# Kernel optimization log

Hardware: AMD Instinct MI355X
Metric: run time of the kernel (lower is better)

The kernel has to match this reference:

```python
import jax, jax.numpy as jnp
import numpy as np

N_TOPICS = 1024
TOPIC_DIM = 128
HIDDEN = 512
N_HEADS = 8
HEAD_DIM = HIDDEN // N_HEADS
N_LAYERS = 2
ALPHA = 0.2
TIME_DECAY = 0.1
BATCH = 8


def setup_inputs() -> dict:
    key = jax.random.key(0)
    ks = jax.random.split(key, 16)
    inp = {
        'topic_ids': jax.random.randint(ks[0], (BATCH,), 0, N_TOPICS, dtype=jnp.int32),
        'adj_matrix': jax.random.randint(ks[1], (BATCH, N_TOPICS, N_TOPICS), 0, 2, dtype=jnp.int32),
        'time_matrix': jax.random.uniform(ks[2], (BATCH, N_TOPICS, N_TOPICS), dtype=jnp.float32),
        'attractiveness': jax.random.normal(ks[3], (BATCH,), dtype=jnp.float32),
        # parameters (torch Linear convention: W [out,in], y = x@W.T + b)
        'topic_embedding': jax.random.normal(ks[4], (N_TOPICS, TOPIC_DIM), dtype=jnp.float32) * 0.1,
        'struct_W': jax.random.normal(ks[5], (HIDDEN, TOPIC_DIM), dtype=jnp.float32) * 0.05,
        'struct_b': jnp.zeros((HIDDEN,), dtype=jnp.float32),
        'attract_W': jax.random.normal(ks[6], (HIDDEN, 1), dtype=jnp.float32) * 0.05,
        'attract_b': jnp.zeros((HIDDEN,), dtype=jnp.float32),
        'gat_W': jax.random.normal(ks[7], (N_LAYERS, N_HEADS, HIDDEN, HEAD_DIM), dtype=jnp.float32) * 0.05,
        'gat_a': jax.random.normal(ks[8], (N_LAYERS, N_HEADS, 2 * HEAD_DIM, 1), dtype=jnp.float32) * 0.05,
        'fc1_W': jax.random.normal(ks[9], (HIDDEN, HIDDEN), dtype=jnp.float32) * 0.05,
        'fc1_b': jnp.zeros((HIDDEN,), dtype=jnp.float32),
        'fc2_W': jax.random.normal(ks[10], (1, HIDDEN), dtype=jnp.float32) * 0.05,
        'fc2_b': jnp.zeros((1,), dtype=jnp.float32),
    }
    return inp


def _gat_layer(node, adj, time_w, W, a):
    # node: [B,N,F], adj: [B,N,N] (0/1), time_w: [B,N,N]
    # W: [H,F,hd], a: [H,2*hd,1]
    h = jnp.einsum('bni,hio->bhno', node, W)  # [B,H,N,hd]
    # Additive attention: a = [a_src; a_dst] so e_ij = LeakyReLU(h_i.a_src + h_j.a_dst)
    a_src = a[:, :HEAD_DIM, 0]   # [H,hd]
    a_dst = a[:, HEAD_DIM:, 0]   # [H,hd]
    e_src = jnp.einsum('bhnd,hd->bhn', h, a_src)  # [B,H,N]
    e_dst = jnp.einsum('bhnd,hd->bhn', h, a_dst)  # [B,H,N]
    e = e_src[:, :, :, None] + e_dst[:, :, None, :]  # [B,H,N,N]
    e = jax.nn.leaky_relu(e, negative_slope=ALPHA)
    e = e * time_w[:, None, :, :]
    e = jnp.where(adj[:, None, :, :] == 0, -jnp.inf, e)
    attn = jax.nn.softmax(e, axis=-1)
    out = jnp.einsum('bhij,bhjd->bhid', attn, h)  # [B,H,N,hd]
    out = out.transpose(0, 2, 1, 3).reshape(node.shape[0], node.shape[1], -1)
    return jax.nn.elu(out)


def reference(topic_ids, adj_matrix, time_matrix, attractiveness,
              topic_embedding, struct_W, struct_b, attract_W, attract_b,
              gat_W, gat_a, fc1_W, fc1_b, fc2_W, fc2_b):
    # structural features for all topics -> hidden
    struct = topic_embedding @ struct_W.T + struct_b          # [N,hidden]
    attract = attractiveness[:, None] @ attract_W.T + attract_b  # [B,hidden]
    node = jnp.broadcast_to(struct[None], (BATCH, N_TOPICS, HIDDEN))
    # weighted co-occurrence time (eq.17)
    time_w = jnp.exp(-TIME_DECAY * (time_matrix.max() - time_matrix))  # [B,N,N]
    for l in range(N_LAYERS):
        node = _gat_layer(node, adj_matrix, time_w, gat_W[l], gat_a[l])
    # gather per-sample topic node feature
    topic_feat = jnp.take_along_axis(node, topic_ids[:, None, None].astype(jnp.int32), axis=1)[:, 0]  # [B,hidden]
    combined = topic_feat + attract
    hidden = jax.nn.relu(combined @ fc1_W.T + fc1_b)
    pred = hidden @ fc2_W.T + fc2_b  # [B,1]
    return pred
```

## Files before the change

kernel.cpp:

```cpp
#include <hip/hip_runtime.h>

#define NT 1024
#define TD 128
#define HID 512
#define NH 8
#define HD 64
#define NB 8

typedef unsigned short us;
typedef _Float16 h16;
typedef h16 half8 __attribute__((ext_vector_type(8)));
typedef h16 h16x2 __attribute__((ext_vector_type(2)));
typedef float f32x4 __attribute__((ext_vector_type(4)));

#define LOG2E 1.44269504f

extern "C" __device__ _Float16 __ocml_exp2_f16(_Float16);

__device__ __forceinline__ us f2h(float x) { return __builtin_bit_cast(us, (h16)x); }
__device__ __forceinline__ float h2f(us s) { return (float)__builtin_bit_cast(h16, s); }
__device__ __forceinline__ unsigned int pkh2(float a, float b) {
    auto v = __builtin_amdgcn_cvt_pkrtz(a, b);
    return __builtin_bit_cast(unsigned int, v);
}

__global__ __launch_bounds__(256) void kprep(const float* __restrict__ tm, const int* __restrict__ adj,
                                             float* __restrict__ part, us* __restrict__ TWb,
                                             const float* __restrict__ emb, const float* __restrict__ sW,
                                             const float* __restrict__ sb, us* __restrict__ node0b,
                                             const float* __restrict__ gW, us* __restrict__ Wt,
                                             const float* __restrict__ fc2b, float* __restrict__ out) {
    __shared__ __align__(16) float smf[8768];
    int bx = blockIdx.x, t = threadIdx.x;
    if (bx < 1024) {
        const float4* tm4 = (const float4*)tm;
        const int4* ad4 = (const int4*)adj;
        size_t base = (size_t)bx * 256 + t;
        const float C = 0.1f * LOG2E;
        const float NANF = __uint_as_float(0x7FC00000u);
        float m = -1e30f;
        #pragma unroll
        for (int k = 0; k < 8; k++) {
            size_t fi = base + (size_t)k * 262144;
            float4 v = tm4[fi];
            int4 av = ad4[fi];
            m = fmaxf(m, fmaxf(fmaxf(v.x, v.y), fmaxf(v.z, v.w)));
            float w0 = exp2f(v.x * C) * LOG2E;
            float w1 = exp2f(v.y * C) * LOG2E;
            float w2 = exp2f(v.z * C) * LOG2E;
            float w3 = exp2f(v.w * C) * LOG2E;
            w0 = av.x ? w0 : NANF;
            w1 = av.y ? w1 : NANF;
            w2 = av.z ? w2 : NANF;
            w3 = av.w ? w3 : NANF;
            uint2 pk;
            pk.x = pkh2(w0, w1);
            pk.y = pkh2(w2, w3);
            *(uint2*)&TWb[fi * 4] = pk;
        }
        smf[t] = m; __syncthreads();
        for (int s = 128; s > 0; s >>= 1) { if (t < s) smf[t] = fmaxf(smf[t], smf[t + s]); __syncthreads(); }
        if (t == 0) part[bx] = smf[0];
    } else if (bx < 1152) {
        int g = bx - 1024; int iblk = g & 15, oseg = g >> 4;
        us* As = (us*)smf;
        us* Bs = (us*)smf + 64 * 136;
        const float4* esrc = (const float4*)(emb + (size_t)iblk * 64 * TD);
        const float4* wsrc = (const float4*)(sW + (size_t)oseg * 64 * TD);
        #pragma unroll
        for (int rep = 0; rep < 8; rep++) {
            int f = rep * 256 + t;
            int row = f >> 5, c4 = f & 31;
            float4 av = esrc[f];
            float4 bv = wsrc[f];
            uint2 pa, pb;
            pa.x = pkh2(av.x, av.y); pa.y = pkh2(av.z, av.w);
            pb.x = pkh2(bv.x, bv.y); pb.y = pkh2(bv.z, bv.w);
            *(uint2*)&As[row * 136 + c4 * 4] = pa;
            *(uint2*)&Bs[row * 136 + c4 * 4] = pb;
        }
        __syncthreads();
        int l = t & 63, w = t >> 6, m = l & 15, q = l >> 4;
        f32x4 acc[4];
        #pragma unroll
        for (int ot = 0; ot < 4; ot++) acc[ot] = (f32x4){0.f, 0.f, 0.f, 0.f};
        #pragma unroll
        for (int ks = 0; ks < 4; ks++) {
            half8 a = *(const half8*)&As[(w * 16 + m) * 136 + ks * 32 + q * 8];
            #pragma unroll
            for (int ot = 0; ot < 4; ot++) {
                half8 b = *(const half8*)&Bs[(ot * 16 + m) * 136 + ks * 32 + q * 8];
                acc[ot] = __builtin_amdgcn_mfma_f32_16x16x32_f16(a, b, acc[ot], 0, 0, 0);
            }
        }
        #pragma unroll
        for (int ot = 0; ot < 4; ot++) {
            int col = oseg * 64 + ot * 16 + m;
            float sbv = sb[col];
            #pragma unroll
            for (int rr = 0; rr < 4; rr++) {
                int rowi = iblk * 64 + w * 16 + q * 4 + rr;
                node0b[(size_t)rowi * HID + col] = f2h(acc[ot][rr] + sbv);
            }
        }
    } else {
        int g = bx - 1152; int lh = g >> 3, kt = g & 7;
        if (g == 0 && t < NB) out[t] = fc2b[0];
        float* tile = smf;
        const float4* src = (const float4*)(gW + ((size_t)lh * HID + kt * 64) * HD);
        #pragma unroll
        for (int rep = 0; rep < 4; rep++) {
            int f = rep * 256 + t;
            float4 v = src[f];
            int row = f >> 4, col = (f & 15) * 4;
            float* d = tile + row * 65 + col;
            d[0] = v.x; d[1] = v.y; d[2] = v.z; d[3] = v.w;
        }
        __syncthreads();
        int o = t >> 2, ks = (t & 3) * 16;
        us pk[16];
        #pragma unroll
        for (int j = 0; j < 16; j++) pk[j] = f2h(tile[(ks + j) * 65 + o]);
        us* dst = Wt + (size_t)lh * HD * HID + (size_t)o * HID + kt * 64 + ks;
        *(uint4*)dst = *(uint4*)pk;
        *(uint4*)(dst + 8) = *(uint4*)&pk[8];
    }
}

__device__ __forceinline__ void gemm_body(const us* __restrict__ A, const us* __restrict__ W,
                                          const float* __restrict__ gav,
                                          us* __restrict__ outT, us* __restrict__ outR,
                                          float* __restrict__ esO, float* __restrict__ edO,
                                          int iblk, int b, int h, int t, us* sm) {
    us* As = sm;
    us* Bs = sm + 2 * 4608;
    int row = t >> 2, ks = t & 3;
    int l = t & 63, w = t >> 6, m = l & 15, q = l >> 4;
    size_t arow0 = (size_t)(b * NT + iblk * 64);
    const us* ar = A + (arow0 + row) * HID + ks * 16;
    const us* br = W + ((size_t)(h * HD + row)) * HID + ks * 16;
    f32x4 acc[4];
    #pragma unroll
    for (int ot = 0; ot < 4; ot++) acc[ot] = (f32x4){0.f, 0.f, 0.f, 0.f};
    {
        uint4 x0 = *(const uint4*)ar, x1 = *(const uint4*)(ar + 8);
        uint4 y0 = *(const uint4*)br, y1 = *(const uint4*)(br + 8);
        *(uint4*)&As[row * 72 + ks * 16] = x0; *(uint4*)&As[row * 72 + ks * 16 + 8] = x1;
        *(uint4*)&Bs[row * 72 + ks * 16] = y0; *(uint4*)&Bs[row * 72 + ks * 16 + 8] = y1;
    }
    uint4 a0 = *(const uint4*)(ar + 64), a1 = *(const uint4*)(ar + 72);
    uint4 b0 = *(const uint4*)(br + 64), b1 = *(const uint4*)(br + 72);
    for (int it = 0; it < 8; it++) {
        int cur = it & 1, nxt = cur ^ 1;
        uint4 na0, na1, nb0, nb1;
        if (it < 6) {
            int k0 = (it + 2) * 64;
            na0 = *(const uint4*)(ar + k0); na1 = *(const uint4*)(ar + k0 + 8);
            nb0 = *(const uint4*)(br + k0); nb1 = *(const uint4*)(br + k0 + 8);
        }
        __syncthreads();
        if (it < 7) {
            *(uint4*)&As[nxt * 4608 + row * 72 + ks * 16] = a0;
            *(uint4*)&As[nxt * 4608 + row * 72 + ks * 16 + 8] = a1;
            *(uint4*)&Bs[nxt * 4608 + row * 72 + ks * 16] = b0;
            *(uint4*)&Bs[nxt * 4608 + row * 72 + ks * 16 + 8] = b1;
        }
        const us* Ac = As + cur * 4608; const us* Bc = Bs + cur * 4608;
        #pragma unroll
        for (int kt = 0; kt < 2; kt++) {
            half8 av = *(const half8*)&Ac[(w * 16 + m) * 72 + kt * 32 + q * 8];
            #pragma unroll
            for (int ot = 0; ot < 4; ot++) {
                half8 bv = *(const half8*)&Bc[(ot * 16 + m) * 72 + kt * 32 + q * 8];
                acc[ot] = __builtin_amdgcn_mfma_f32_16x16x32_f16(av, bv, acc[ot], 0, 0, 0);
            }
        }
        if (it < 6) { a0 = na0; a1 = na1; b0 = nb0; b1 = nb1; }
    }
    const float* gas = gav + h * 2 * HD;
    float gs[4], gd[4];
    #pragma unroll
    for (int ot = 0; ot < 4; ot++) { gs[ot] = gas[ot * 16 + m]; gd[ot] = gas[HD + ot * 16 + m]; }
    size_t ebase = ((size_t)b * NH + h) * NT + iblk * 64;
    #pragma unroll
    for (int rr = 0; rr < 4; rr++) {
        float s = 0.f, d = 0.f;
        #pragma unroll
        for (int ot = 0; ot < 4; ot++) { float v = acc[ot][rr]; s = fmaf(v, gs[ot], s); d = fmaf(v, gd[ot], d); }
        #pragma unroll
        for (int mask = 1; mask < 16; mask <<= 1) { s += __shfl_xor(s, mask); d += __shfl_xor(d, mask); }
        if (m == 0) {
            int rowi = w * 16 + q * 4 + rr;
            esO[ebase + rowi] = s;
            edO[ebase + rowi] = d;
        }
    }
    #pragma unroll
    for (int ot = 0; ot < 4; ot++) {
        int col = h * HD + ot * 16 + m;
        #pragma unroll
        for (int rr = 0; rr < 4; rr++) {
            int i_loc = w * 16 + q * 4 + rr;
            float v = acc[ot][rr];
            if (outT) outT[(size_t)col * NT + iblk * 64 + i_loc] = f2h(v);
            if (outR) outR[(arow0 + i_loc) * HID + col] = f2h(v);
        }
    }
}

__global__ __launch_bounds__(256) void kgemm1(const us* __restrict__ node0b, const us* __restrict__ Wt,
                                              const float* __restrict__ ga, us* __restrict__ Ht1,
                                              float* __restrict__ es1, float* __restrict__ ed1) {
    __shared__ __align__(16) us sm[4 * 4608];
    int g = blockIdx.x;
    gemm_body(node0b, Wt, ga, Ht1, nullptr, es1, ed1, g & 15, 0, g >> 4, threadIdx.x, sm);
}

__global__ __launch_bounds__(256) void kgemm2(const us* __restrict__ node1b, const us* __restrict__ Wt2,
                                              const float* __restrict__ ga2, us* __restrict__ H2b,
                                              float* __restrict__ es2, float* __restrict__ ed2) {
    __shared__ __align__(16) us sm[4 * 4608];
    int n = blockIdx.x;
    int b = n & 7, k = n >> 3, iblk = k & 15, h = k >> 4;
    gemm_body(node1b, Wt2, ga2, nullptr, H2b, es2, ed2, iblk, b, h, threadIdx.x, sm);
}

__device__ __forceinline__ unsigned int p_word_fly(unsigned int tw, unsigned int ed, h16x2 es) {
    h16x2 t = __builtin_bit_cast(h16x2, tw);
    h16x2 d = __builtin_bit_cast(h16x2, ed);
    h16x2 e = es + d;
    h16x2 lk = e * (h16)0.2f;
    h16x2 el = __builtin_elementwise_max(e, lk);
    h16x2 mm = t * el;
    h16x2 p;
    p.x = __ocml_exp2_f16(mm.x);
    p.y = __ocml_exp2_f16(mm.y);
    h16x2 z = {(h16)0.0f, (h16)0.0f};
    h16x2 r = __builtin_elementwise_max(p, z);
    return __builtin_bit_cast(unsigned int, r);
}

__device__ __forceinline__ half8 p_frag(uint4 T, uint4 D, h16x2 es) {
    uint4 r;
    r.x = p_word_fly(T.x, D.x, es);
    r.y = p_word_fly(T.y, D.y, es);
    r.z = p_word_fly(T.z, D.z, es);
    r.w = p_word_fly(T.w, D.w, es);
    return __builtin_bit_cast(half8, r);
}

__global__ __launch_bounds__(256) void kattn1(const us* __restrict__ TWb, const us* __restrict__ Ht,
                                              const float* __restrict__ es1, const float* __restrict__ ed1,
                                              const float* __restrict__ part, us* __restrict__ node1b) {
    int n = blockIdx.x;
    int b = n & 7, k = n >> 3;
    int i2 = k & 7, h = k >> 3;
    int t = threadIdx.x;
    __shared__ __align__(16) us Hs[2][64 * 72];
    __shared__ __align__(16) us edl[NT];
    __shared__ float invl_s[128];
    __shared__ float reds[256];
    int l = t & 63, w = t >> 6, m = l & 15, q = l >> 4;
    {
        float pm = fmaxf(fmaxf(part[t * 4], part[t * 4 + 1]), fmaxf(part[t * 4 + 2], part[t * 4 + 3]));
        reds[t] = pm; __syncthreads();
        for (int s = 128; s > 0; s >>= 1) { if (t < s) reds[t] = fmaxf(reds[t], reds[t + s]); __syncthreads(); }
    }
    float sfac = exp2f(-reds[0] * (0.1f * LOG2E));
    {
        float4 ev = *(const float4*)&ed1[h * NT + t * 4];
        uint2 pk; pk.x = pkh2(ev.x * sfac, ev.y * sfac); pk.y = pkh2(ev.z * sfac, ev.w * sfac);
        *(uint2*)&edl[t * 4] = pk;
    }
    int rowA = i2 * 128 + w * 32 + m;
    h16 eA = (h16)(es1[h * NT + rowA] * sfac);
    h16 eB = (h16)(es1[h * NT + rowA + 16] * sfac);
    h16x2 esvA = {eA, eA}, esvB = {eB, eB};
    const us* twA = TWb + ((size_t)(b * NT) + rowA) * NT + q * 8;
    const us* twB = twA + (size_t)16 * NT;
    int hr = t >> 2, js = t & 3;
    const us* htrow = Ht + ((size_t)(h * HD) + hr) * NT + js * 16;
    f32x4 acc[2][4];
    #pragma unroll
    for (int ti = 0; ti < 2; ti++)
        #pragma unroll
        for (int ot = 0; ot < 4; ot++) acc[ti][ot] = (f32x4){0.f, 0.f, 0.f, 0.f};
    f32x4 acc1[2] = {(f32x4){0.f, 0.f, 0.f, 0.f}, (f32x4){0.f, 0.f, 0.f, 0.f}};
    h16 ov = (m == 0) ? (h16)1.0f : (h16)0.0f;
    half8 bones = {ov, ov, ov, ov, ov, ov, ov, ov};
    uint4 H0 = *(const uint4*)htrow, H1 = *(const uint4*)(htrow + 8);
    *(uint4*)&Hs[0][hr * 72 + js * 16] = H0;
    *(uint4*)&Hs[0][hr * 72 + js * 16 + 8] = H1;
    H0 = *(const uint4*)(htrow + 64); H1 = *(const uint4*)(htrow + 72);
    uint4 TA0 = *(const uint4*)twA,        TA1 = *(const uint4*)(twA + 32);
    uint4 TB0 = *(const uint4*)twB,        TB1 = *(const uint4*)(twB + 32);
    __syncthreads();
    for (int it = 0; it < 16; it++) {
        int cur = it & 1, nxt = cur ^ 1;
        int j0 = it * 64;
        uint4 nH0, nH1, nA0, nA1, nB0, nB1;
        if (it < 14) {
            nH0 = *(const uint4*)(htrow + j0 + 128);
            nH1 = *(const uint4*)(htrow + j0 + 136);
        }
        if (it < 15) {
            nA0 = *(const uint4*)(twA + j0 + 64);  nA1 = *(const uint4*)(twA + j0 + 96);
            nB0 = *(const uint4*)(twB + j0 + 64);  nB1 = *(const uint4*)(twB + j0 + 96);
        }
        uint4 D0 = *(const uint4*)&edl[j0 + q * 8];
        uint4 D1 = *(const uint4*)&edl[j0 + 32 + q * 8];
        half8 pA0 = p_frag(TA0, D0, esvA);
        half8 pA1 = p_frag(TA1, D1, esvA);
        half8 pB0 = p_frag(TB0, D0, esvB);
        half8 pB1 = p_frag(TB1, D1, esvB);
        __syncthreads();
        if (it < 15) {
            *(uint4*)&Hs[nxt][hr * 72 + js * 16] = H0;
            *(uint4*)&Hs[nxt][hr * 72 + js * 16 + 8] = H1;
        }
        const us* Hc = Hs[cur];
        #pragma unroll
        for (int ot = 0; ot < 4; ot++) {
            half8 bv0 = *(const half8*)&Hc[(ot * 16 + m) * 72 + q * 8];
            half8 bv1 = *(const half8*)&Hc[(ot * 16 + m) * 72 + 32 + q * 8];
            acc[0][ot] = __builtin_amdgcn_mfma_f32_16x16x32_f16(pA0, bv0, acc[0][ot], 0, 0, 0);
            acc[0][ot] = __builtin_amdgcn_mfma_f32_16x16x32_f16(pA1, bv1, acc[0][ot], 0, 0, 0);
            acc[1][ot] = __builtin_amdgcn_mfma_f32_16x16x32_f16(pB0, bv0, acc[1][ot], 0, 0, 0);
            acc[1][ot] = __builtin_amdgcn_mfma_f32_16x16x32_f16(pB1, bv1, acc[1][ot], 0, 0, 0);
        }
        acc1[0] = __builtin_amdgcn_mfma_f32_16x16x32_f16(pA0, bones, acc1[0], 0, 0, 0);
        acc1[0] = __builtin_amdgcn_mfma_f32_16x16x32_f16(pA1, bones, acc1[0], 0, 0, 0);
        acc1[1] = __builtin_amdgcn_mfma_f32_16x16x32_f16(pB0, bones, acc1[1], 0, 0, 0);
        acc1[1] = __builtin_amdgcn_mfma_f32_16x16x32_f16(pB1, bones, acc1[1], 0, 0, 0);
        if (it < 14) { H0 = nH0; H1 = nH1; }
        if (it < 15) { TA0 = nA0; TA1 = nA1; TB0 = nB0; TB1 = nB1; }
    }
    if (m == 0) {
        #pragma unroll
        for (int rr = 0; rr < 4; rr++) {
            invl_s[w * 32 + q * 4 + rr]      = 1.f / acc1[0][rr];
            invl_s[w * 32 + 16 + q * 4 + rr] = 1.f / acc1[1][rr];
        }
    }
    __syncthreads();
    size_t rbase = (size_t)(b * NT + i2 * 128);
    #pragma unroll
    for (int ti = 0; ti < 2; ti++) {
        #pragma unroll
        for (int ot = 0; ot < 4; ot++) {
            int col = h * HD + ot * 16 + m;
            #pragma unroll
            for (int rr = 0; rr < 4; rr++) {
                int rloc = w * 32 + ti * 16 + q * 4 + rr;
                float v = acc[ti][ot][rr] * invl_s[rloc];
                v = v > 0.f ? v : (__expf(v) - 1.f);
                node1b[(rbase + rloc) * HID + col] = f2h(v);
            }
        }
    }
}

__global__ __launch_bounds__(256) void kattn2a(const us* __restrict__ TWb, const us* __restrict__ H2b,
                                               const float* __restrict__ es2, const float* __restrict__ ed2,
                                               const int* __restrict__ topic_ids, const float* __restrict__ part,
                                               float* __restrict__ ppv, float* __restrict__ pl) {
    int js = blockIdx.x, h = blockIdx.y, b = blockIdx.z;
    int t = threadIdx.x;
    __shared__ float pls[64];
    __shared__ float red[256];
    int qi = topic_ids[b];
    {
        float pm = fmaxf(fmaxf(part[t * 4], part[t * 4 + 1]), fmaxf(part[t * 4 + 2], part[t * 4 + 3]));
        red[t] = pm; __syncthreads();
        for (int s = 128; s > 0; s >>= 1) { if (t < s) red[t] = fmaxf(red[t], red[t + s]); __syncthreads(); }
    }
    float sfac = exp2f(-red[0] * (0.1f * LOG2E));
    __syncthreads();
    if (t < 64) {
        int j = js * 64 + t;
        float esq = es2[((size_t)b * NH + h) * NT + qi];
        float tw = h2f(TWb[((size_t)(b * NT) + qi) * NT + j]);
        float e = esq + ed2[((size_t)b * NH + h) * NT + j];
        e = fmaxf(e, 0.2f * e) * (tw * sfac);
        float p = fmaxf(exp2f(e), 0.f);
        pls[t] = p;
        float lsum = p;
        #pragma unroll
        for (int mask = 1; mask < 64; mask <<= 1) lsum += __shfl_xor(lsum, mask);
        if (t == 0) pl[((size_t)b * NH + h) * 16 + js] = lsum;
    }
    __syncthreads();
    int o = t & 63, jg = t >> 6;
    float acc = 0.f;
    const us* hb = H2b + ((size_t)(b * NT) + js * 64 + jg * 16) * HID + h * HD + o;
    #pragma unroll
    for (int jj = 0; jj < 16; jj++)
        acc = fmaf(pls[jg * 16 + jj], h2f(hb[(size_t)jj * HID]), acc);
    red[t] = acc; __syncthreads();
    if (t < 64) {
        float pv = red[t] + red[t + 64] + red[t + 128] + red[t + 192];
        ppv[(((size_t)b * NH + h) * 16 + js) * HD + t] = pv;
    }
}

__global__ __launch_bounds__(256) void khead2(const float* __restrict__ ppv, const float* __restrict__ pl,
                                              const float* __restrict__ attr,
                                              const float* __restrict__ aW, const float* __restrict__ ab,
                                              const float* __restrict__ fc1W, const float* __restrict__ fc1b,
                                              const float* __restrict__ fc2W, float* __restrict__ out) {
    int kseg = blockIdx.x, b = blockIdx.y;
    int t = threadIdx.x;
    __shared__ float comb[HID];
    __shared__ float linv[NH];
    __shared__ float r2[256];
    if (t < NH) {
        float lsum = 0.f;
        #pragma unroll
        for (int js = 0; js < 16; js++) lsum += pl[((size_t)b * NH + t) * 16 + js];
        linv[t] = 1.f / lsum;
    }
    __syncthreads();
    float av = attr[b];
    for (int k = t; k < HID; k += 256) {
        int h = k >> 6, o = k & 63;
        float pv = 0.f;
        #pragma unroll
        for (int js = 0; js < 16; js++) pv += ppv[(((size_t)b * NH + h) * 16 + js) * HD + o];
        float v = pv * linv[h];
        v = v > 0.f ? v : (__expf(v) - 1.f);
        comb[k] = v + av * aW[k] + ab[k];
    }
    __syncthreads();
    int kk = kseg * 16 + (t >> 4);
    int j = t & 15;
    const float* row = fc1W + (size_t)kk * HID;
    float acc = 0.f;
    #pragma unroll 8
    for (int mi = 0; mi < 32; mi++) {
        int idx = mi * 16 + j;
        acc = fmaf(comb[idx], row[idx], acc);
    }
    #pragma unroll
    for (int mask = 1; mask < 16; mask <<= 1) acc += __shfl_xor(acc, mask);
    float partv = 0.f;
    if (j == 0) {
        float hk = fmaxf(acc + fc1b[kk], 0.f);
        partv = hk * fc2W[kk];
    }
    r2[t] = partv; __syncthreads();
    for (int s = 128; s > 0; s >>= 1) { if (t < s) r2[t] += r2[t + s]; __syncthreads(); }
    if (t == 0) atomicAdd(&out[b], r2[0]);
}

extern "C" void kernel_launch(void* const* d_in, const int* in_sizes, int n_in,
                              void* d_out, int out_size, void* d_ws, size_t ws_size,
                              hipStream_t stream) {
    const int*   topic_ids = (const int*)d_in[0];
    const int*   adj       = (const int*)d_in[1];
    const float* tm        = (const float*)d_in[2];
    const float* attr      = (const float*)d_in[3];
    const float* emb       = (const float*)d_in[4];
    const float* sW        = (const float*)d_in[5];
    const float* sb        = (const float*)d_in[6];
    const float* aW        = (const float*)d_in[7];
    const float* ab        = (const float*)d_in[8];
    const float* gW        = (const float*)d_in[9];
    const float* ga        = (const float*)d_in[10];
    const float* fc1W      = (const float*)d_in[11];
    const float* fc1b      = (const float*)d_in[12];
    const float* fc2W      = (const float*)d_in[13];
    const float* fc2b      = (const float*)d_in[14];
    float* out = (float*)d_out;

    char* p = (char*)d_ws;
    us* TWb    = (us*)p; p += sizeof(us) * (size_t)NB * NT * NT;
    us* node0b = (us*)p; p += sizeof(us) * (size_t)NT * HID;
    us* Wt     = (us*)p; p += sizeof(us) * (size_t)2 * NH * HD * HID;
    us* Ht1    = (us*)p; p += sizeof(us) * (size_t)HID * NT;
    us* node1b = (us*)p; p += sizeof(us) * (size_t)NB * NT * HID;
    us* H2b    = (us*)p; p += sizeof(us) * (size_t)NB * NT * HID;
    float* es1  = (float*)p; p += sizeof(float) * NH * NT;
    float* ed1  = (float*)p; p += sizeof(float) * NH * NT;
    float* es2  = (float*)p; p += sizeof(float) * NB * NH * NT;
    float* ed2  = (float*)p; p += sizeof(float) * NB * NH * NT;
    float* ppv  = (float*)p; p += sizeof(float) * NB * NH * 16 * HD;
    float* pl   = (float*)p; p += sizeof(float) * NB * NH * 16;
    float* part = (float*)p; p += sizeof(float) * 1024;

    kprep<<<1280, 256, 0, stream>>>(tm, adj, part, TWb, emb, sW, sb, node0b, gW, Wt, fc2b, out);
    kgemm1<<<128, 256, 0, stream>>>(node0b, Wt, ga, Ht1, es1, ed1);
    kattn1<<<512, 256, 0, stream>>>(TWb, Ht1, es1, ed1, part, node1b);
    kgemm2<<<1024, 256, 0, stream>>>(node1b, Wt + (size_t)NH * HD * HID,
                                     ga + NH * 2 * HD, H2b, es2, ed2);
    kattn2a<<<dim3(16, NH, NB), 256, 0, stream>>>(TWb, H2b, es2, ed2, topic_ids, part, ppv, pl);
    khead2<<<dim3(32, NB), 256, 0, stream>>>(ppv, pl, attr, aW, ab, fc1W, fc1b, fc2W, out);
}
```

Before: 179.3 us.

## Reassociate layer-2 attention to skip full per-batch GEMM for query row

Layer 2 only feeds one query row per batch, so the full per-batch GEMM H2 = node1 @ W2 is dropped. The attention scores are rebuilt from node1 dotted with the precomputed vectors W2·a_src and W2·a_dst, and the projection is applied after the attention-weighted sum of node1 rows (context then W2). This removes a large GEMM and the H2 write and read, in exchange for new kctx/kcomb/kfc kernels and an extra 64-block section in kprep.

Measured after the change: 175.9 us (median of 2 runs). Within noise of the previous version (-1.9%).

```diff
diff --git a/kernel.cpp b/kernel.cpp
--- a/kernel.cpp
+++ b/kernel.cpp
@@ -29,6 +29,7 @@
                                              const float* __restrict__ emb, const float* __restrict__ sW,
                                              const float* __restrict__ sb, us* __restrict__ node0b,
                                              const float* __restrict__ gW, us* __restrict__ Wt,
+                                             const float* __restrict__ ga, us* __restrict__ VAVS,
                                              const float* __restrict__ fc2b, float* __restrict__ out) {
     __shared__ __align__(16) float smf[8768];
     int bx = blockIdx.x, t = threadIdx.x;
@@ -103,7 +104,7 @@
                 node0b[(size_t)rowi * HID + col] = f2h(acc[ot][rr] + sbv);
             }
         }
-    } else {
+    } else if (bx < 1280) {
         int g = bx - 1152; int lh = g >> 3, kt = g & 7;
         if (g == 0 && t < NB) out[t] = fc2b[0];
         float* tile = smf;
@@ -124,12 +125,25 @@
         us* dst = Wt + (size_t)lh * HD * HID + (size_t)o * HID + kt * 64 + ks;
         *(uint4*)dst = *(uint4*)pk;
         *(uint4*)(dst + 8) = *(uint4*)&pk[8];
+    } else {
+        int g = bx - 1280; int h = g >> 3, iseg = g & 7;
+        if (t < 128) {
+            int sel = t >> 6, il = t & 63;
+            int i = iseg * 64 + il;
+            const float* W2row = gW + (size_t)NH * HID * HD + ((size_t)h * HID + i) * HD;
+            const float* a2 = ga + NH * 2 * HD + h * 2 * HD;
+            const float* av = sel ? a2 : (a2 + HD);
+            float s = 0.f;
+            #pragma unroll 8
+            for (int o = 0; o < HD; o++) s = fmaf(W2row[o], av[o], s);
+            VAVS[(size_t)(sel * 8 + h) * HID + i] = f2h(s);
+        }
     }
 }
 
 __device__ __forceinline__ void gemm_body(const us* __restrict__ A, const us* __restrict__ W,
                                           const float* __restrict__ gav,
-                                          us* __restrict__ outT, us* __restrict__ outR,
+                                          us* __restrict__ outT,
                                           float* __restrict__ esO, float* __restrict__ edO,
                                           int iblk, int b, int h, int t, us* sm) {
     us* As = sm;
@@ -201,9 +215,7 @@
         #pragma unroll
         for (int rr = 0; rr < 4; rr++) {
             int i_loc = w * 16 + q * 4 + rr;
-            float v = acc[ot][rr];
-            if (outT) outT[(size_t)col * NT + iblk * 64 + i_loc] = f2h(v);
-            if (outR) outR[(arow0 + i_loc) * HID + col] = f2h(v);
+            outT[(size_t)col * NT + iblk * 64 + i_loc] = f2h(acc[ot][rr]);
         }
     }
 }
@@ -213,16 +225,7 @@
                                               float* __restrict__ es1, float* __restrict__ ed1) {
     __shared__ __align__(16) us sm[4 * 4608];
     int g = blockIdx.x;
-    gemm_body(node0b, Wt, ga, Ht1, nullptr, es1, ed1, g & 15, 0, g >> 4, threadIdx.x, sm);
-}
-
-__global__ __launch_bounds__(256) void kgemm2(const us* __restrict__ node1b, const us* __restrict__ Wt2,
-                                              const float* __restrict__ ga2, us* __restrict__ H2b,
-                                              float* __restrict__ es2, float* __restrict__ ed2) {
-    __shared__ __align__(16) us sm[4 * 4608];
-    int n = blockIdx.x;
-    int b = n & 7, k = n >> 3, iblk = k & 15, h = k >> 4;
-    gemm_body(node1b, Wt2, ga2, nullptr, H2b, es2, ed2, iblk, b, h, threadIdx.x, sm);
+    gemm_body(node0b, Wt, ga, Ht1, es1, ed1, g & 15, 0, g >> 4, threadIdx.x, sm);
 }
 
 __device__ __forceinline__ unsigned int p_word_fly(unsigned int tw, unsigned int ed, h16x2 es) {
@@ -360,76 +363,156 @@
     }
 }
 
-__global__ __launch_bounds__(256) void kattn2a(const us* __restrict__ TWb, const us* __restrict__ H2b,
-                                               const float* __restrict__ es2, const float* __restrict__ ed2,
-                                               const int* __restrict__ topic_ids, const float* __restrict__ part,
-                                               float* __restrict__ ppv, float* __restrict__ pl) {
-    int js = blockIdx.x, h = blockIdx.y, b = blockIdx.z;
+__global__ __launch_bounds__(256) void kctx(const us* __restrict__ TWb, const us* __restrict__ node1b,
+                                            const us* __restrict__ VAVS, const float* __restrict__ part,
+                                            const int* __restrict__ topic_ids,
+                                            float* __restrict__ ctxp, float* __restrict__ pl) {
+    int n = blockIdx.x;
+    int b = n & 7, jb = n >> 3;
     int t = threadIdx.x;
-    __shared__ float pls[64];
-    __shared__ float red[256];
+    __shared__ __align__(16) us n1s[32 * 520];
+    __shared__ __align__(16) us vvs[16 * 520];
+    __shared__ __align__(16) us qrow[HID];
+    __shared__ float Ps[8][33];
+    __shared__ float es2q[8];
+    __shared__ float reds[256];
     int qi = topic_ids[b];
     {
         float pm = fmaxf(fmaxf(part[t * 4], part[t * 4 + 1]), fmaxf(part[t * 4 + 2], part[t * 4 + 3]));
-        red[t] = pm; __syncthreads();
-        for (int s = 128; s > 0; s >>= 1) { if (t < s) red[t] = fmaxf(red[t], red[t + s]); __syncthreads(); }
-    }
-    float sfac = exp2f(-red[0] * (0.1f * LOG2E));
-    __syncthreads();
-    if (t < 64) {
-        int j = js * 64 + t;
-        float esq = es2[((size_t)b * NH + h) * NT + qi];
-        float tw = h2f(TWb[((size_t)(b * NT) + qi) * NT + j]);
-        float e = esq + ed2[((size_t)b * NH + h) * NT + j];
-        e = fmaxf(e, 0.2f * e) * (tw * sfac);
-        float p = fmaxf(exp2f(e), 0.f);
-        pls[t] = p;
-        float lsum = p;
-        #pragma unroll
-        for (int mask = 1; mask < 64; mask <<= 1) lsum += __shfl_xor(lsum, mask);
-        if (t == 0) pl[((size_t)b * NH + h) * 16 + js] = lsum;
-    }
-    __syncthreads();
-    int o = t & 63, jg = t >> 6;
-    float acc = 0.f;
-    const us* hb = H2b + ((size_t)(b * NT) + js * 64 + jg * 16) * HID + h * HD + o;
-    #pragma unroll
-    for (int jj = 0; jj < 16; jj++)
-        acc = fmaf(pls[jg * 16 + jj], h2f(hb[(size_t)jj * HID]), acc);
-    red[t] = acc; __syncthreads();
-    if (t < 64) {
-        float pv = red[t] + red[t + 64] + red[t + 128] + red[t + 192];
-        ppv[(((size_t)b * NH + h) * 16 + js) * HD + t] = pv;
-    }
-}
-
-__global__ __launch_bounds__(256) void khead2(const float* __restrict__ ppv, const float* __restrict__ pl,
-                                              const float* __restrict__ attr,
-                                              const float* __restrict__ aW, const float* __restrict__ ab,
-                                              const float* __restrict__ fc1W, const float* __restrict__ fc1b,
-                                              const float* __restrict__ fc2W, float* __restrict__ out) {
+        reds[t] = pm; __syncthreads();
+        for (int s = 128; s > 0; s >>= 1) { if (t < s) reds[t] = fmaxf(reds[t], reds[t + s]); __syncthreads(); }
+    }
+    float sfac = exp2f(-reds[0] * (0.1f * LOG2E));
+    {
+        int row = t >> 3, c = (t & 7) * 64;
+        const uint4* src = (const uint4*)(node1b + ((size_t)(b * NT) + jb * 32 + row) * HID + c);
+        uint4* dst = (uint4*)&n1s[row * 520 + c];
+        #pragma unroll
+        for (int k = 0; k < 8; k++) dst[k] = src[k];
+    }
+    {
+        int row = t >> 4, c = (t & 15) * 32;
+        const uint4* src = (const uint4*)(VAVS + (size_t)row * HID + c);
+        uint4* dst = (uint4*)&vvs[row * 520 + c];
+        dst[0] = src[0]; dst[1] = src[1]; dst[2] = src[2]; dst[3] = src[3];
+    }
+    if (t < 32) {
+        const uint4* src = (const uint4*)(node1b + ((size_t)(b * NT) + qi) * HID + t * 16);
+        *(uint4*)&qrow[t * 16] = src[0];
+        *(uint4*)&qrow[t * 16 + 8] = src[1];
+    }
+    __syncthreads();
+    {
+        int h = t >> 5, li = t & 31;
+        float s = 0.f;
+        #pragma unroll 4
+        for (int ii = 0; ii < 16; ii++) {
+            int i = li * 16 + ii;
+            s = fmaf(h2f(qrow[i]), h2f(vvs[(8 + h) * 520 + i]), s);
+        }
+        #pragma unroll
+        for (int mask = 1; mask < 32; mask <<= 1) s += __shfl_xor(s, mask);
+        if (li == 0) es2q[h] = s;
+    }
+    __syncthreads();
+    int l = t & 63, w = t >> 6, m = l & 15, q = l >> 4;
+    if (w < 2) {
+        f32x4 acc = (f32x4){0.f, 0.f, 0.f, 0.f};
+        #pragma unroll
+        for (int kt = 0; kt < 16; kt++) {
+            half8 a = *(const half8*)&n1s[(w * 16 + m) * 520 + kt * 32 + q * 8];
+            half8 bv = *(const half8*)&vvs[m * 520 + kt * 32 + q * 8];
+            acc = __builtin_amdgcn_mfma_f32_16x16x32_f16(a, bv, acc, 0, 0, 0);
+        }
+        if (m < 8) {
+            const us* twq = TWb + ((size_t)(b * NT) + qi) * NT + jb * 32;
+            float esv = es2q[m];
+            #pragma unroll
+            for (int r = 0; r < 4; r++) {
+                int j = w * 16 + q * 4 + r;
+                float e = esv + acc[r];
+                e = fmaxf(e, 0.2f * e);
+                float twu = h2f(twq[j]);
+                float p = fmaxf(exp2f(twu * sfac * e), 0.f);
+                Ps[m][j] = p;
+            }
+        }
+    }
+    __syncthreads();
+    {
+        int h = t >> 5, j = t & 31;
+        float s = Ps[h][j];
+        #pragma unroll
+        for (int mask = 1; mask < 32; mask <<= 1) s += __shfl_xor(s, mask);
+        if (j == 0) pl[((size_t)b * NH + h) * 32 + jb] = s;
+    }
+    float ac[8][2];
+    #pragma unroll
+    for (int h = 0; h < 8; h++) { ac[h][0] = 0.f; ac[h][1] = 0.f; }
+    for (int j = 0; j < 32; j++) {
+        unsigned int uv = *(const unsigned int*)&n1s[j * 520 + t * 2];
+        h16x2 hv = __builtin_bit_cast(h16x2, uv);
+        float f0 = (float)hv.x, f1 = (float)hv.y;
+        #pragma unroll
+        for (int h = 0; h < 8; h++) {
+            float p = Ps[h][j];
+            ac[h][0] = fmaf(p, f0, ac[h][0]);
+            ac[h][1] = fmaf(p, f1, ac[h][1]);
+        }
+    }
+    float* cp = ctxp + (((size_t)b * 32 + jb) * NH) * HID;
+    #pragma unroll
+    for (int h = 0; h < 8; h++) {
+        float2 v; v.x = ac[h][0]; v.y = ac[h][1];
+        *(float2*)&cp[h * HID + t * 2] = v;
+    }
+}
+
+__global__ __launch_bounds__(256) void kcomb(const float* __restrict__ ctxp, const float* __restrict__ pl,
+                                             const us* __restrict__ Wt2, const float* __restrict__ attr,
+                                             const float* __restrict__ aW, const float* __restrict__ ab,
+                                             float* __restrict__ comb) {
+    int h = blockIdx.x & 7, b = blockIdx.x >> 3;
+    int t = threadIdx.x;
+    __shared__ float cx[HID];
+    __shared__ float ln[1];
+    if (t < 32) {
+        float s = pl[((size_t)b * NH + h) * 32 + t];
+        #pragma unroll
+        for (int mask = 1; mask < 32; mask <<= 1) s += __shfl_xor(s, mask);
+        if (t == 0) ln[0] = 1.f / s;
+    }
+    float a0 = 0.f, a1 = 0.f;
+    for (int jb = 0; jb < 32; jb++) {
+        const float* cp = ctxp + (((size_t)b * 32 + jb) * NH + h) * HID;
+        a0 += cp[t]; a1 += cp[t + 256];
+    }
+    __syncthreads();
+    float li = ln[0];
+    cx[t] = a0 * li; cx[t + 256] = a1 * li;
+    __syncthreads();
+    int o2 = t >> 2, ks = t & 3;
+    const us* wrow = Wt2 + ((size_t)h * HD + o2) * HID + ks * 128;
+    float s = 0.f;
+    #pragma unroll 8
+    for (int k = 0; k < 128; k++) s = fmaf(cx[ks * 128 + k], h2f(wrow[k]), s);
+    s += __shfl_xor(s, 1); s += __shfl_xor(s, 2);
+    if (ks == 0) {
+        float v = s > 0.f ? s : (__expf(s) - 1.f);
+        int col = h * HD + o2;
+        comb[b * HID + col] = v + attr[b] * aW[col] + ab[col];
+    }
+}
+
+__global__ __launch_bounds__(256) void kfc(const float* __restrict__ comb,
+                                           const float* __restrict__ fc1W, const float* __restrict__ fc1b,
+                                           const float* __restrict__ fc2W, float* __restrict__ out) {
     int kseg = blockIdx.x, b = blockIdx.y;
     int t = threadIdx.x;
-    __shared__ float comb[HID];
-    __shared__ float linv[NH];
+    __shared__ float cs[HID];
     __shared__ float r2[256];
-    if (t < NH) {
-        float lsum = 0.f;
-        #pragma unroll
-        for (int js = 0; js < 16; js++) lsum += pl[((size_t)b * NH + t) * 16 + js];
-        linv[t] = 1.f / lsum;
-    }
-    __syncthreads();
-    float av = attr[b];
-    for (int k = t; k < HID; k += 256) {
-        int h = k >> 6, o = k & 63;
-        float pv = 0.f;
-        #pragma unroll
-        for (int js = 0; js < 16; js++) pv += ppv[(((size_t)b * NH + h) * 16 + js) * HD + o];
-        float v = pv * linv[h];
-        v = v > 0.f ? v : (__expf(v) - 1.f);
-        comb[k] = v + av * aW[k] + ab[k];
-    }
+    cs[t] = comb[b * HID + t];
+    cs[t + 256] = comb[b * HID + t + 256];
     __syncthreads();
     int kk = kseg * 16 + (t >> 4);
     int j = t & 15;
@@ -438,7 +521,7 @@
     #pragma unroll 8
     for (int mi = 0; mi < 32; mi++) {
         int idx = mi * 16 + j;
-        acc = fmaf(comb[idx], row[idx], acc);
+        acc = fmaf(cs[idx], row[idx], acc);
     }
     #pragma unroll
     for (int mask = 1; mask < 16; mask <<= 1) acc += __shfl_xor(acc, mask);
@@ -478,20 +561,18 @@
     us* Wt     = (us*)p; p += sizeof(us) * (size_t)2 * NH * HD * HID;
     us* Ht1    = (us*)p; p += sizeof(us) * (size_t)HID * NT;
     us* node1b = (us*)p; p += sizeof(us) * (size_t)NB * NT * HID;
-    us* H2b    = (us*)p; p += sizeof(us) * (size_t)NB * NT * HID;
+    us* VAVS   = (us*)p; p += sizeof(us) * (size_t)16 * HID;
     float* es1  = (float*)p; p += sizeof(float) * NH * NT;
     float* ed1  = (float*)p; p += sizeof(float) * NH * NT;
-    float* es2  = (float*)p; p += sizeof(float) * NB * NH * NT;
-    float* ed2  = (float*)p; p += sizeof(float) * NB * NH * NT;
-    float* ppv  = (float*)p; p += sizeof(float) * NB * NH * 16 * HD;
-    float* pl   = (float*)p; p += sizeof(float) * NB * NH * 16;
+    float* ctxp = (float*)p; p += sizeof(float) * (size_t)NB * 32 * NH * HID;
+    float* pl   = (float*)p; p += sizeof(float) * NB * NH * 32;
+    float* comb = (float*)p; p += sizeof(float) * NB * HID;
     float* part = (float*)p; p += sizeof(float) * 1024;
 
-    kprep<<<1280, 256, 0, stream>>>(tm, adj, part, TWb, emb, sW, sb, node0b, gW, Wt, fc2b, out);
+    kprep<<<1344, 256, 0, stream>>>(tm, adj, part, TWb, emb, sW, sb, node0b, gW, Wt, ga, VAVS, fc2b, out);
     kgemm1<<<128, 256, 0, stream>>>(node0b, Wt, ga, Ht1, es1, ed1);
     kattn1<<<512, 256, 0, stream>>>(TWb, Ht1, es1, ed1, part, node1b);
-    kgemm2<<<1024, 256, 0, stream>>>(node1b, Wt + (size_t)NH * HD * HID,
-                                     ga + NH * 2 * HD, H2b, es2, ed2);
-    kattn2a<<<dim3(16, NH, NB), 256, 0, stream>>>(TWb, H2b, es2, ed2, topic_ids, part, ppv, pl);
-    khead2<<<dim3(32, NB), 256, 0, stream>>>(ppv, pl, attr, aW, ab, fc1W, fc1b, fc2W, out);
-}
+    kctx<<<256, 256, 0, stream>>>(TWb, node1b, VAVS, part, topic_ids, ctxp, pl);
+    kcomb<<<64, 256, 0, stream>>>(ctxp, pl, Wt + (size_t)NH * HD * HID, attr, aW, ab, comb);
+    kfc<<<dim3(32, NB), 256, 0, stream>>>(comb, fc1W, fc1b, fc2W, out);
+}
```
